# Optimization experiments

Hardware: AMD Instinct MI355X
Metric: run time of the kernel (lower is better)

The kernel has to match this reference:

```python
import jax, jax.numpy as jnp
import numpy as np

NUM_HEADS = 16
SPAN = 256  # pos_ebd_size (position_buckets)


def _split_heads(x, num_heads):
    # x: (B, S, D) -> (B*num_heads, S, D//num_heads)
    b, s, d = x.shape
    return x.reshape(b, s, num_heads, d // num_heads).transpose(0, 2, 1, 3).reshape(b * num_heads, s, d // num_heads)


def setup_inputs() -> dict:
    key = jax.random.key(0)
    ks = jax.random.split(key, 12)
    B, S, D = 1, 2048, 1024
    std = 0.02
    n_src = NUM_HEADS * S * 2 * SPAN   # flat size of c2p/p2c score tensor
    n_dst = NUM_HEADS * S * S          # flat size of gathered bias
    return {
        "hidden_states": jax.random.normal(ks[0], (B, S, D), jnp.float32),
        "rel_embeddings": jax.random.normal(ks[1], (2 * SPAN, D), jnp.float32),
        "Wq": jax.random.normal(ks[2], (D, D), jnp.float32) * std,
        "bq": jnp.zeros((D,), jnp.float32),
        "Wk": jax.random.normal(ks[3], (D, D), jnp.float32) * std,
        "bk": jnp.zeros((D,), jnp.float32),
        "Wv": jax.random.normal(ks[4], (D, D), jnp.float32) * std,
        "bv": jnp.zeros((D,), jnp.float32),
        "ids": jax.random.randint(ks[5], (n_dst,), 0, n_src, jnp.int32),
        "ids_t": jax.random.randint(ks[6], (n_dst,), 0, n_src, jnp.int32),
    }


def reference(hidden_states, rel_embeddings, Wq, bq, Wk, bk, Wv, bv, ids, ids_t):
    B, S, D = hidden_states.shape
    dh = D // NUM_HEADS
    # pos_att_type = ['c2p','p2c'] -> scale_factor = 3
    scale = jnp.sqrt(jnp.asarray(dh * 3, jnp.float32))

    q = _split_heads(hidden_states @ Wq + bq, NUM_HEADS)  # (B*H, S, dh)
    k = _split_heads(hidden_states @ Wk + bk, NUM_HEADS)
    v = _split_heads(hidden_states @ Wv + bv, NUM_HEADS)

    scores = jnp.einsum('bsd,btd->bst', q, k) / scale  # (B*H, S, S)

    # share_att_key=True: reuse key/query projections on relative embeddings
    pos = rel_embeddings[: 2 * SPAN][None]             # (1, 2*SPAN, D)
    pos_k = _split_heads(pos @ Wk + bk, NUM_HEADS)     # (H, 2*SPAN, dh)
    pos_q = _split_heads(pos @ Wq + bq, NUM_HEADS)

    bs = q.shape[0]  # == H when B == 1 (required by the original bmm)
    # c2p: gather from flattened (bs, S, 2*SPAN) scores
    c2p = jnp.einsum('bsd,bkd->bsk', q, pos_k)
    c2p_bias = c2p.reshape(-1)[ids].reshape(bs, S, S) / scale
    # p2c: gather then transpose last two dims
    p2c = jnp.einsum('bsd,bkd->bsk', k, pos_q)
    p2c_bias = jnp.swapaxes(p2c.reshape(-1)[ids_t].reshape(bs, S, S), -1, -2) / scale

    scores = scores + c2p_bias + p2c_bias
    probs = jax.nn.softmax(scores, axis=-1)
    ctx = jnp.einsum('bst,btd->bsd', probs, v)         # (B*H, S, dh)
    ctx = ctx.reshape(B, NUM_HEADS, S, dh).transpose(0, 2, 1, 3).reshape(B, S, D)
    return ctx
```

## Files before the change

kernel.cpp:

```cpp
#include <hip/hip_runtime.h>
#include <math.h>

#define S_LEN 2048
#define D_DIM 1024
#define NH 16
#define DH 64
#define NPOS 512

__global__ __launch_bounds__(256) void proj_gemm(
    const float* __restrict__ X, const float* __restrict__ W,
    const float* __restrict__ bias, float* __restrict__ outp, int M) {
  __shared__ float xt[16][132];
  __shared__ float wt[16][128];
  const int tid = threadIdx.x;
  const int br = blockIdx.y, bc = blockIdx.x;
  const int r0 = (tid >> 4) * 8, c0 = (tid & 15) * 8;
  float acc[8][8];
  #pragma unroll
  for (int i = 0; i < 8; i++)
    #pragma unroll
    for (int j = 0; j < 8; j++) acc[i][j] = 0.f;

  const float* Xb = X + (size_t)br * 128 * D_DIM;
  const float* Wb = W + bc * 128;

  for (int k0 = 0; k0 < D_DIM; k0 += 16) {
    __syncthreads();
    #pragma unroll
    for (int i = 0; i < 2; i++) {
      int slot = tid + i * 256;
      int row = slot >> 2;
      int kc = (slot & 3) * 4;
      float4 xv = *(const float4*)(Xb + (size_t)row * D_DIM + k0 + kc);
      xt[kc + 0][row] = xv.x; xt[kc + 1][row] = xv.y;
      xt[kc + 2][row] = xv.z; xt[kc + 3][row] = xv.w;
      int kr = slot >> 5;
      int wc = (slot & 31) * 4;
      *(float4*)&wt[kr][wc] = *(const float4*)(Wb + (size_t)(k0 + kr) * D_DIM + wc);
    }
    __syncthreads();
    #pragma unroll
    for (int kk = 0; kk < 16; kk++) {
      float a[8], b[8];
      *(float4*)&a[0] = *(const float4*)&xt[kk][r0];
      *(float4*)&a[4] = *(const float4*)&xt[kk][r0 + 4];
      *(float4*)&b[0] = *(const float4*)&wt[kk][c0];
      *(float4*)&b[4] = *(const float4*)&wt[kk][c0 + 4];
      #pragma unroll
      for (int ii = 0; ii < 8; ii++)
        #pragma unroll
        for (int jj = 0; jj < 8; jj++)
          acc[ii][jj] = fmaf(a[ii], b[jj], acc[ii][jj]);
    }
  }

  const int n0 = bc * 128 + c0;
  const int h = n0 >> 6, iw = n0 & 63;
  float bvals[8];
  #pragma unroll
  for (int jj = 0; jj < 8; jj++) bvals[jj] = bias[n0 + jj];
  #pragma unroll
  for (int ii = 0; ii < 8; ii++) {
    size_t row = (size_t)br * 128 + r0 + ii;
    float ov[8];
    #pragma unroll
    for (int jj = 0; jj < 8; jj++) ov[jj] = acc[ii][jj] + bvals[jj];
    float* dst = outp + ((size_t)h * M + row) * 64 + iw;
    *(float4*)dst = *(float4*)&ov[0];
    *(float4*)(dst + 4) = *(float4*)&ov[4];
  }
}

__global__ __launch_bounds__(256) void rel_gemm(
    const float* __restrict__ q_ws, const float* __restrict__ k_ws,
    const float* __restrict__ pk_ws, const float* __restrict__ pq_ws,
    float* __restrict__ c2p, float* __restrict__ p2c, float inv_scale) {
  __shared__ float at[16][132];
  __shared__ float bt[16][132];
  const int tid = threadIdx.x;
  const int h = blockIdx.z & 15;
  const int which = blockIdx.z >> 4;
  const float* A = (which ? k_ws : q_ws) + (size_t)h * S_LEN * DH;
  const float* Bm = (which ? pq_ws : pk_ws) + (size_t)h * NPOS * DH;
  float* C = (which ? p2c : c2p) + (size_t)h * S_LEN * NPOS;
  const int br = blockIdx.y, bc = blockIdx.x;
  const int r0 = (tid >> 4) * 8, c0 = (tid & 15) * 8;
  float acc[8][8];
  #pragma unroll
  for (int i = 0; i < 8; i++)
    #pragma unroll
    for (int j = 0; j < 8; j++) acc[i][j] = 0.f;

  for (int k0 = 0; k0 < DH; k0 += 16) {
    __syncthreads();
    #pragma unroll
    for (int i = 0; i < 2; i++) {
      int slot = tid + i * 256;
      int row = slot >> 2;
      int kc = (slot & 3) * 4;
      float4 av = *(const float4*)(A + (size_t)(br * 128 + row) * DH + k0 + kc);
      at[kc + 0][row] = av.x; at[kc + 1][row] = av.y;
      at[kc + 2][row] = av.z; at[kc + 3][row] = av.w;
      float4 bv = *(const float4*)(Bm + (size_t)(bc * 128 + row) * DH + k0 + kc);
      bt[kc + 0][row] = bv.x; bt[kc + 1][row] = bv.y;
      bt[kc + 2][row] = bv.z; bt[kc + 3][row] = bv.w;
    }
    __syncthreads();
    #pragma unroll
    for (int kk = 0; kk < 16; kk++) {
      float a[8], b[8];
      *(float4*)&a[0] = *(const float4*)&at[kk][r0];
      *(float4*)&a[4] = *(const float4*)&at[kk][r0 + 4];
      *(float4*)&b[0] = *(const float4*)&bt[kk][c0];
      *(float4*)&b[4] = *(const float4*)&bt[kk][c0 + 4];
      #pragma unroll
      for (int ii = 0; ii < 8; ii++)
        #pragma unroll
        for (int jj = 0; jj < 8; jj++)
          acc[ii][jj] = fmaf(a[ii], b[jj], acc[ii][jj]);
    }
  }
  #pragma unroll
  for (int ii = 0; ii < 8; ii++) {
    size_t row = (size_t)br * 128 + r0 + ii;
    float ov[8];
    #pragma unroll
    for (int jj = 0; jj < 8; jj++) ov[jj] = acc[ii][jj] * inv_scale;
    float* dst = C + row * NPOS + bc * 128 + c0;
    *(float4*)dst = *(float4*)&ov[0];
    *(float4*)(dst + 4) = *(float4*)&ov[4];
  }
}

__global__ __launch_bounds__(256) void attn_kernel(
    const float* __restrict__ q_ws, const float* __restrict__ k_ws,
    const float* __restrict__ v_ws, const float* __restrict__ c2p,
    const float* __restrict__ p2c, const int* __restrict__ ids,
    const int* __restrict__ ids_t, float* __restrict__ outp, float inv_scale) {
  __shared__ float qT[64][68];
  __shared__ float kT[64][68];
  __shared__ float vS[64][64];
  const int tid = threadIdx.x;
  const int h = blockIdx.y;
  const int s0 = blockIdx.x * 64;
  const int r4 = tid >> 4, c4 = tid & 15;
  const int r0 = r4 * 4, c0 = c4 * 4;

  const float* qb = q_ws + ((size_t)h * S_LEN + s0) * DH;
  const float* kb = k_ws + (size_t)h * S_LEN * DH;
  const float* vb = v_ws + (size_t)h * S_LEN * DH;

  #pragma unroll
  for (int i = 0; i < 4; i++) {
    int slot = tid + i * 256;
    int s = slot >> 4;
    int dc = (slot & 15) * 4;
    float4 qv = *(const float4*)(qb + (size_t)s * DH + dc);
    qT[dc + 0][s] = qv.x; qT[dc + 1][s] = qv.y;
    qT[dc + 2][s] = qv.z; qT[dc + 3][s] = qv.w;
  }

  float m[4], l[4], o[4][4];
  #pragma unroll
  for (int ii = 0; ii < 4; ii++) {
    m[ii] = -INFINITY; l[ii] = 0.f;
    #pragma unroll
    for (int jj = 0; jj < 4; jj++) o[ii][jj] = 0.f;
  }

  for (int kt = 0; kt < S_LEN / 64; kt++) {
    const int t0 = kt * 64;
    __syncthreads();
    #pragma unroll
    for (int i = 0; i < 4; i++) {
      int slot = tid + i * 256;
      int t = slot >> 4;
      int dc = (slot & 15) * 4;
      float4 kv = *(const float4*)(kb + (size_t)(t0 + t) * DH + dc);
      kT[dc + 0][t] = kv.x; kT[dc + 1][t] = kv.y;
      kT[dc + 2][t] = kv.z; kT[dc + 3][t] = kv.w;
      float4 vv = *(const float4*)(vb + (size_t)(t0 + t) * DH + dc);
      *(float4*)&vS[t][dc] = vv;
    }
    __syncthreads();

    float sc[4][4];
    #pragma unroll
    for (int ii = 0; ii < 4; ii++)
      #pragma unroll
      for (int jj = 0; jj < 4; jj++) sc[ii][jj] = 0.f;
    #pragma unroll 8
    for (int d = 0; d < 64; d++) {
      float a[4], b[4];
      *(float4*)a = *(const float4*)&qT[d][r0];
      *(float4*)b = *(const float4*)&kT[d][c0];
      #pragma unroll
      for (int ii = 0; ii < 4; ii++)
        #pragma unroll
        for (int jj = 0; jj < 4; jj++)
          sc[ii][jj] = fmaf(a[ii], b[jj], sc[ii][jj]);
    }
    #pragma unroll
    for (int ii = 0; ii < 4; ii++)
      #pragma unroll
      for (int jj = 0; jj < 4; jj++) sc[ii][jj] *= inv_scale;

    #pragma unroll
    for (int ii = 0; ii < 4; ii++) {
      const size_t s = s0 + r0 + ii;
      int4 iv = *(const int4*)(ids + ((size_t)h * S_LEN + s) * S_LEN + t0 + c0);
      sc[ii][0] += c2p[iv.x]; sc[ii][1] += c2p[iv.y];
      sc[ii][2] += c2p[iv.z]; sc[ii][3] += c2p[iv.w];
    }
    #pragma unroll
    for (int jj = 0; jj < 4; jj++) {
      const size_t t = t0 + c0 + jj;
      int4 iv = *(const int4*)(ids_t + ((size_t)h * S_LEN + t) * S_LEN + s0 + r0);
      sc[0][jj] += p2c[iv.x]; sc[1][jj] += p2c[iv.y];
      sc[2][jj] += p2c[iv.z]; sc[3][jj] += p2c[iv.w];
    }

    #pragma unroll
    for (int ii = 0; ii < 4; ii++) {
      float v = fmaxf(fmaxf(sc[ii][0], sc[ii][1]), fmaxf(sc[ii][2], sc[ii][3]));
      v = fmaxf(v, __shfl_xor(v, 1));
      v = fmaxf(v, __shfl_xor(v, 2));
      v = fmaxf(v, __shfl_xor(v, 4));
      v = fmaxf(v, __shfl_xor(v, 8));
      float mn = fmaxf(m[ii], v);
      float alpha = __expf(m[ii] - mn);
      m[ii] = mn;
      float rs = 0.f;
      #pragma unroll
      for (int jj = 0; jj < 4; jj++) {
        sc[ii][jj] = __expf(sc[ii][jj] - mn);
        rs += sc[ii][jj];
      }
      rs += __shfl_xor(rs, 1);
      rs += __shfl_xor(rs, 2);
      rs += __shfl_xor(rs, 4);
      rs += __shfl_xor(rs, 8);
      l[ii] = l[ii] * alpha + rs;
      #pragma unroll
      for (int jj = 0; jj < 4; jj++) o[ii][jj] *= alpha;
    }

    __syncthreads();
    #pragma unroll
    for (int jj = 0; jj < 4; jj++) {
      float pv[4] = {sc[0][jj], sc[1][jj], sc[2][jj], sc[3][jj]};
      *(float4*)&kT[c0 + jj][r0] = *(float4*)pv;
    }
    __syncthreads();

    #pragma unroll 8
    for (int t = 0; t < 64; t++) {
      float a[4], b[4];
      *(float4*)a = *(const float4*)&kT[t][r0];
      *(float4*)b = *(const float4*)&vS[t][c0];
      #pragma unroll
      for (int ii = 0; ii < 4; ii++)
        #pragma unroll
        for (int jj = 0; jj < 4; jj++)
          o[ii][jj] = fmaf(a[ii], b[jj], o[ii][jj]);
    }
  }

  #pragma unroll
  for (int ii = 0; ii < 4; ii++) {
    float inv_l = 1.0f / l[ii];
    float ov[4];
    #pragma unroll
    for (int jj = 0; jj < 4; jj++) ov[jj] = o[ii][jj] * inv_l;
    float* dst = outp + (size_t)(s0 + r0 + ii) * D_DIM + h * DH + c0;
    *(float4*)dst = *(float4*)ov;
  }
}

extern "C" void kernel_launch(void* const* d_in, const int* in_sizes, int n_in,
                              void* d_out, int out_size, void* d_ws, size_t ws_size,
                              hipStream_t stream) {
  const float* hs  = (const float*)d_in[0];
  const float* rel = (const float*)d_in[1];
  const float* Wq  = (const float*)d_in[2];
  const float* bq  = (const float*)d_in[3];
  const float* Wk  = (const float*)d_in[4];
  const float* bk  = (const float*)d_in[5];
  const float* Wv  = (const float*)d_in[6];
  const float* bv  = (const float*)d_in[7];
  const int* ids   = (const int*)d_in[8];
  const int* ids_t = (const int*)d_in[9];
  float* outp = (float*)d_out;

  float* ws = (float*)d_ws;
  float* q_ws  = ws;
  float* k_ws  = q_ws + 2097152;
  float* v_ws  = k_ws + 2097152;
  float* pk_ws = v_ws + 2097152;
  float* pq_ws = pk_ws + 524288;
  float* c2p_ws = pq_ws + 524288;
  float* p2c_ws = c2p_ws + 16777216;

  const float inv_scale = 1.0f / sqrtf((float)(DH * 3));

  dim3 blk(256);
  proj_gemm<<<dim3(8, 16), blk, 0, stream>>>(hs, Wq, bq, q_ws, S_LEN);
  proj_gemm<<<dim3(8, 16), blk, 0, stream>>>(hs, Wk, bk, k_ws, S_LEN);
  proj_gemm<<<dim3(8, 16), blk, 0, stream>>>(hs, Wv, bv, v_ws, S_LEN);
  proj_gemm<<<dim3(8, 4),  blk, 0, stream>>>(rel, Wk, bk, pk_ws, NPOS);
  proj_gemm<<<dim3(8, 4),  blk, 0, stream>>>(rel, Wq, bq, pq_ws, NPOS);
  rel_gemm<<<dim3(4, 16, 32), blk, 0, stream>>>(q_ws, k_ws, pk_ws, pq_ws,
                                                c2p_ws, p2c_ws, inv_scale);
  attn_kernel<<<dim3(32, 16), blk, 0, stream>>>(q_ws, k_ws, v_ws, c2p_ws,
                                                p2c_ws, ids, ids_t, outp, inv_scale);
}
```

Measured before the change: 3.577 ms.

## Halve attention query tile to 32 rows and use nontemporal index loads

The attention kernel now processes 32 query rows per block instead of 64, doubling the grid to 1024 blocks so more work is in flight on the many CUs. Each thread computes a 2x4 score tile, and the P tile is stored in kT with a 34-float stride. The index streams (ids, ids_t) are read with nontemporal loads and the output is written with nontemporal stores so they do not pollute cache used by the c2p/p2c gather tables. In exchange, each block reloads K and V for only half as many queries, doubling K/V traffic, and the ids_t loads shrink to 8-byte reads.

```diff
diff --git a/kernel.cpp b/kernel.cpp
--- a/kernel.cpp
+++ b/kernel.cpp
@@ -6,6 +6,10 @@
 #define NH 16
 #define DH 64
 #define NPOS 512
+
+typedef int   vi4 __attribute__((ext_vector_type(4)));
+typedef int   vi2 __attribute__((ext_vector_type(2)));
+typedef float vf4 __attribute__((ext_vector_type(4)));
 
 __global__ __launch_bounds__(256) void proj_gemm(
     const float* __restrict__ X, const float* __restrict__ W,
@@ -137,21 +141,23 @@
     const float* __restrict__ v_ws, const float* __restrict__ c2p,
     const float* __restrict__ p2c, const int* __restrict__ ids,
     const int* __restrict__ ids_t, float* __restrict__ outp, float inv_scale) {
-  __shared__ float qT[64][68];
+  __shared__ float qT[64][36];
   __shared__ float kT[64][68];
   __shared__ float vS[64][64];
   const int tid = threadIdx.x;
   const int h = blockIdx.y;
-  const int s0 = blockIdx.x * 64;
-  const int r4 = tid >> 4, c4 = tid & 15;
-  const int r0 = r4 * 4, c0 = c4 * 4;
+  const int s0 = blockIdx.x * 32;
+  const int rg = tid >> 4, cg = tid & 15;
+  const int r0 = rg * 2, c0 = cg * 4;
 
   const float* qb = q_ws + ((size_t)h * S_LEN + s0) * DH;
   const float* kb = k_ws + (size_t)h * S_LEN * DH;
   const float* vb = v_ws + (size_t)h * S_LEN * DH;
-
-  #pragma unroll
-  for (int i = 0; i < 4; i++) {
+  const int* idsb  = ids   + (size_t)h * S_LEN * S_LEN;
+  const int* idstb = ids_t + (size_t)h * S_LEN * S_LEN;
+
+  #pragma unroll
+  for (int i = 0; i < 2; i++) {
     int slot = tid + i * 256;
     int s = slot >> 4;
     int dc = (slot & 15) * 4;
@@ -160,9 +166,9 @@
     qT[dc + 2][s] = qv.z; qT[dc + 3][s] = qv.w;
   }
 
-  float m[4], l[4], o[4][4];
-  #pragma unroll
-  for (int ii = 0; ii < 4; ii++) {
+  float m[2], l[2], o[2][4];
+  #pragma unroll
+  for (int ii = 0; ii < 2; ii++) {
     m[ii] = -INFINITY; l[ii] = 0.f;
     #pragma unroll
     for (int jj = 0; jj < 4; jj++) o[ii][jj] = 0.f;
@@ -184,44 +190,43 @@
     }
     __syncthreads();
 
-    float sc[4][4];
-    #pragma unroll
-    for (int ii = 0; ii < 4; ii++)
+    float sc[2][4];
+    #pragma unroll
+    for (int ii = 0; ii < 2; ii++)
       #pragma unroll
       for (int jj = 0; jj < 4; jj++) sc[ii][jj] = 0.f;
     #pragma unroll 8
     for (int d = 0; d < 64; d++) {
-      float a[4], b[4];
-      *(float4*)a = *(const float4*)&qT[d][r0];
-      *(float4*)b = *(const float4*)&kT[d][c0];
-      #pragma unroll
-      for (int ii = 0; ii < 4; ii++)
-        #pragma unroll
-        for (int jj = 0; jj < 4; jj++)
-          sc[ii][jj] = fmaf(a[ii], b[jj], sc[ii][jj]);
-    }
-    #pragma unroll
-    for (int ii = 0; ii < 4; ii++)
+      float2 a = *(const float2*)&qT[d][r0];
+      float4 b = *(const float4*)&kT[d][c0];
+      sc[0][0] = fmaf(a.x, b.x, sc[0][0]); sc[0][1] = fmaf(a.x, b.y, sc[0][1]);
+      sc[0][2] = fmaf(a.x, b.z, sc[0][2]); sc[0][3] = fmaf(a.x, b.w, sc[0][3]);
+      sc[1][0] = fmaf(a.y, b.x, sc[1][0]); sc[1][1] = fmaf(a.y, b.y, sc[1][1]);
+      sc[1][2] = fmaf(a.y, b.z, sc[1][2]); sc[1][3] = fmaf(a.y, b.w, sc[1][3]);
+    }
+    #pragma unroll
+    for (int ii = 0; ii < 2; ii++)
       #pragma unroll
       for (int jj = 0; jj < 4; jj++) sc[ii][jj] *= inv_scale;
 
     #pragma unroll
-    for (int ii = 0; ii < 4; ii++) {
-      const size_t s = s0 + r0 + ii;
-      int4 iv = *(const int4*)(ids + ((size_t)h * S_LEN + s) * S_LEN + t0 + c0);
+    for (int ii = 0; ii < 2; ii++) {
+      const int s = s0 + r0 + ii;
+      vi4 iv = __builtin_nontemporal_load(
+          (const vi4*)(idsb + (size_t)s * S_LEN + t0 + c0));
       sc[ii][0] += c2p[iv.x]; sc[ii][1] += c2p[iv.y];
       sc[ii][2] += c2p[iv.z]; sc[ii][3] += c2p[iv.w];
     }
     #pragma unroll
     for (int jj = 0; jj < 4; jj++) {
-      const size_t t = t0 + c0 + jj;
-      int4 iv = *(const int4*)(ids_t + ((size_t)h * S_LEN + t) * S_LEN + s0 + r0);
+      const int t = t0 + c0 + jj;
+      vi2 iv = __builtin_nontemporal_load(
+          (const vi2*)(idstb + (size_t)t * S_LEN + s0 + r0));
       sc[0][jj] += p2c[iv.x]; sc[1][jj] += p2c[iv.y];
-      sc[2][jj] += p2c[iv.z]; sc[3][jj] += p2c[iv.w];
-    }
-
-    #pragma unroll
-    for (int ii = 0; ii < 4; ii++) {
+    }
+
+    #pragma unroll
+    for (int ii = 0; ii < 2; ii++) {
       float v = fmaxf(fmaxf(sc[ii][0], sc[ii][1]), fmaxf(sc[ii][2], sc[ii][3]));
       v = fmaxf(v, __shfl_xor(v, 1));
       v = fmaxf(v, __shfl_xor(v, 2));
@@ -246,34 +251,32 @@
     }
 
     __syncthreads();
+    float* pT = &kT[0][0];
     #pragma unroll
     for (int jj = 0; jj < 4; jj++) {
-      float pv[4] = {sc[0][jj], sc[1][jj], sc[2][jj], sc[3][jj]};
-      *(float4*)&kT[c0 + jj][r0] = *(float4*)pv;
+      float2 pv = make_float2(sc[0][jj], sc[1][jj]);
+      *(float2*)(pT + (size_t)(c0 + jj) * 34 + r0) = pv;
     }
     __syncthreads();
 
     #pragma unroll 8
     for (int t = 0; t < 64; t++) {
-      float a[4], b[4];
-      *(float4*)a = *(const float4*)&kT[t][r0];
-      *(float4*)b = *(const float4*)&vS[t][c0];
-      #pragma unroll
-      for (int ii = 0; ii < 4; ii++)
-        #pragma unroll
-        for (int jj = 0; jj < 4; jj++)
-          o[ii][jj] = fmaf(a[ii], b[jj], o[ii][jj]);
-    }
-  }
-
-  #pragma unroll
-  for (int ii = 0; ii < 4; ii++) {
+      float2 a = *(const float2*)(pT + (size_t)t * 34 + r0);
+      float4 b = *(const float4*)&vS[t][c0];
+      o[0][0] = fmaf(a.x, b.x, o[0][0]); o[0][1] = fmaf(a.x, b.y, o[0][1]);
+      o[0][2] = fmaf(a.x, b.z, o[0][2]); o[0][3] = fmaf(a.x, b.w, o[0][3]);
+      o[1][0] = fmaf(a.y, b.x, o[1][0]); o[1][1] = fmaf(a.y, b.y, o[1][1]);
+      o[1][2] = fmaf(a.y, b.z, o[1][2]); o[1][3] = fmaf(a.y, b.w, o[1][3]);
+    }
+  }
+
+  #pragma unroll
+  for (int ii = 0; ii < 2; ii++) {
     float inv_l = 1.0f / l[ii];
-    float ov[4];
-    #pragma unroll
-    for (int jj = 0; jj < 4; jj++) ov[jj] = o[ii][jj] * inv_l;
-    float* dst = outp + (size_t)(s0 + r0 + ii) * D_DIM + h * DH + c0;
-    *(float4*)dst = *(float4*)ov;
+    vf4 ov = { o[ii][0] * inv_l, o[ii][1] * inv_l,
+               o[ii][2] * inv_l, o[ii][3] * inv_l };
+    __builtin_nontemporal_store(
+        ov, (vf4*)(outp + (size_t)(s0 + r0 + ii) * D_DIM + h * DH + c0));
   }
 }
 
@@ -311,6 +314,6 @@
   proj_gemm<<<dim3(8, 4),  blk, 0, stream>>>(rel, Wq, bq, pq_ws, NPOS);
   rel_gemm<<<dim3(4, 16, 32), blk, 0, stream>>>(q_ws, k_ws, pk_ws, pq_ws,
                                                 c2p_ws, p2c_ws, inv_scale);
-  attn_kernel<<<dim3(32, 16), blk, 0, stream>>>(q_ws, k_ws, v_ws, c2p_ws,
+  attn_kernel<<<dim3(64, 16), blk, 0, stream>>>(q_ws, k_ws, v_ws, c2p_ws,
                                                 p2c_ws, ids, ids_t, outp, inv_scale);
 }
```

After: 3.642 ms. No clear change (+1.8%).
